# Performance work log

Hardware: AMD Instinct MI355X
Metric: run time of the kernel (lower is better)

Reference implementation:

```python
import jax, jax.numpy as jnp
import numpy as np

VEC_DIM = 64
RANK = 2


def setup_inputs() -> dict:
    key = jax.random.key(0)
    kg, km, kp = jax.random.split(key, 3)
    grid = jax.random.normal(kg, (193, 193, VEC_DIM), dtype=jnp.float32)
    # nn.init.uniform_(M.weight, -0.5, 0.5)
    M_weight = jax.random.uniform(km, (VEC_DIM, VEC_DIM), minval=-0.5, maxval=0.5, dtype=jnp.float32)
    # nn.init.uniform_(P, -0.1, 0.1)
    P = jax.random.uniform(kp, (VEC_DIM, VEC_DIM), minval=-0.1, maxval=0.1, dtype=jnp.float32)
    return {"grid": grid, "M_weight": M_weight, "P": P}


def reference(grid, M_weight, P):
    H, W, m = grid.shape
    # periods1[i,j] = periods2[i,j] = i*m + j + 2
    periods = (jnp.arange(m, dtype=jnp.float32)[:, None] * m
               + jnp.arange(m, dtype=jnp.float32)[None, :] + 2.0)  # [m, m]

    # ---- window extraction: linear mode (step=1), rank_mode='drop', rank_op='avg' ----
    nH = H - RANK + 1
    nW = W - RANK + 1
    win_sum = jax.lax.reduce_window(grid, 0.0, jax.lax.add,
                                    (RANK, RANK, 1), (1, 1, 1), 'VALID')  # [nH, nW, m]
    x_win = (win_sum / float(RANK * RANK)).reshape(nH * nW, m)  # [B, m]

    # ---- map through M (nn.Linear, no bias): y = x @ W^T ----
    x = x_win @ M_weight.T  # [B, m]

    # ---- phi_table gather: phi[k1,k2] = cos(2*pi*k1/periods) * cos(2*pi*k2/periods) ----
    two_pi = jnp.float32(2.0 * np.pi)
    k1s = jnp.arange(nH, dtype=jnp.float32)
    k2s = jnp.arange(nW, dtype=jnp.float32)
    cos1 = jnp.cos(two_pi * k1s[:, None, None] / periods)  # [nH, m, m]
    cos2 = jnp.cos(two_pi * k2s[:, None, None] / periods)  # [nW, m, m]
    phi = (cos1[:, None, :, :] * cos2[None, :, :, :]).reshape(nH * nW, m, m)  # [B, m, m]

    # ---- Nk = einsum('bj,ij,bij->bi', x, P, phi) ----
    Nk = jnp.einsum('bj,ij,bij->bi', x, P, phi)  # [B, m]
    return Nk
```

## Files before the change

kernel.cpp:

```cpp
#include <hip/hip_runtime.h>
#include <math.h>

#define NH 192
#define NW 192
#define Wt 193
#define TG 24
#define NTILE (TG*TG)
#define TILE_SZ 4096
#define TBLK 3072

__device__ __forceinline__ float cos_rev(float num, float den) {
    float rev = num * __builtin_amdgcn_rcpf(den);
    rev = __builtin_amdgcn_fractf(rev);
    return __builtin_amdgcn_cosf(rev);
}

__global__ __launch_bounds__(256) void k_prep(const float* __restrict__ grid,
                                              const float* __restrict__ Mw,
                                              const float* __restrict__ P,
                                              float* __restrict__ Cz,
                                              float* __restrict__ CP1,
                                              float* __restrict__ xt) {
    __shared__ float Ms[64 * 64];
    __shared__ float win[64 * 68];
    int bx = blockIdx.x;
    int t = threadIdx.x;

    if (bx < TBLK) {
        int idx = bx * 256 + t;
        int r  = idx & 3;
        int i  = (idx >> 2) & 63;
        int kg = (idx >> 8) % 48;
        int j  = idx / 12288;
        int k  = kg * 4 + r;
        Cz[idx] = cos_rev((float)k, (float)(i * 64 + j + 2));
        int i2 = idx & 63;
        int k2 = (idx >> 6) % 192;
        int j2 = idx / 12288;
        int t2 = i2 * 64 + j2;
        CP1[idx] = cos_rev((float)k2, (float)(t2 + 2)) * P[t2];
        return;
    }

    int bb = bx - TBLK;
    int k1g = bb % TG, k2g = bb / TG;

    #pragma unroll
    for (int r = 0; r < 4; ++r) {
        int e = r * 256 + t;
        ((float4*)Ms)[e] = ((const float4*)Mw)[e];
    }

    {
        int c = t & 63, pq = t >> 6;
        const float* gb = grid + ((size_t)(k1g * 8) * Wt + k2g * 8) * 64;
        #pragma unroll
        for (int r = 0; r < 16; ++r) {
            int p = pq * 16 + r;
            int l1 = p >> 3, l2 = p & 7;
            const float* g0 = gb + ((size_t)l1 * Wt + l2) * 64;
            float s = g0[c] + g0[64 + c] + g0[Wt * 64 + c] + g0[Wt * 64 + 64 + c];
            win[p * 68 + c] = 0.25f * s;
        }
    }
    __syncthreads();

    int p = t & 63, jq = t >> 6;
    float4 wv[16];
    #pragma unroll
    for (int q = 0; q < 16; ++q) wv[q] = *(const float4*)&win[p * 68 + 4 * q];

    float* xb = xt + (size_t)(k1g * TG + k2g) * TILE_SZ;
    #pragma unroll
    for (int r = 0; r < 16; ++r) {
        int j = jq * 16 + r;
        float acc = 0.f;
        #pragma unroll
        for (int q = 0; q < 16; ++q) {
            float4 mv = *(const float4*)&Ms[j * 64 + 4 * q];
            acc += wv[q].x * mv.x + wv[q].y * mv.y + wv[q].z * mv.z + wv[q].w * mv.w;
        }
        xb[(size_t)j * 64 + p] = acc;
    }
}

__global__ __launch_bounds__(512) void k_main(const float* __restrict__ xt,
                                              const float* __restrict__ Cz,
                                              const float* __restrict__ CP1,
                                              float* __restrict__ out) {
    __shared__ float4 cs[2048];
    int bx = blockIdx.x;
    int k1g = bx % TG, k2g = bx / TG;
    int t = threadIdx.x;
    int lane = t & 63;
    int w = __builtin_amdgcn_readfirstlane(t >> 6);
    int k1 = k1g * 8 + w;

    const float*  c1p = CP1 + (size_t)k1 * 64 + lane;
    const float*  xb  = xt + (size_t)(k1g * TG + k2g) * TILE_SZ + w * 8;
    const float4* Cz4 = (const float4*)Cz;
    int kgb = k2g * 2;

    float acc[8];
    #pragma unroll
    for (int l2 = 0; l2 < 8; ++l2) acc[l2] = 0.f;

    for (int jc = 0; jc < 4; ++jc) {
        __syncthreads();
        #pragma unroll
        for (int r = 0; r < 4; ++r) {
            int e = r * 512 + t;
            int jj = e >> 7;
            int g  = (e >> 6) & 1;
            int i  = e & 63;
            cs[e] = Cz4[(size_t)((jc * 16 + jj) * 48 + kgb + g) * 64 + i];
        }
        __syncthreads();

        #pragma unroll 4
        for (int jj = 0; jj < 16; ++jj) {
            int j = jc * 16 + jj;
            float  c1 = c1p[(size_t)j * 12288];
            float4 v0 = cs[jj * 128 + lane];
            float4 v1 = cs[jj * 128 + 64 + lane];
            const float4* xj = (const float4*)(xb + (size_t)j * 64);
            float4 x0 = xj[0];
            float4 x1 = xj[1];
            float c2f[8] = {v0.x, v0.y, v0.z, v0.w, v1.x, v1.y, v1.z, v1.w};
            float xs[8]  = {x0.x, x0.y, x0.z, x0.w, x1.x, x1.y, x1.z, x1.w};
            #pragma unroll
            for (int l2 = 0; l2 < 8; ++l2)
                acc[l2] += xs[l2] * (c1 * c2f[l2]);
        }
    }

    size_t ob = ((size_t)k1 * NW + k2g * 8) * 64 + lane;
    #pragma unroll
    for (int l2 = 0; l2 < 8; ++l2)
        out[ob + (size_t)l2 * 64] = acc[l2];
}

extern "C" void kernel_launch(void* const* d_in, const int* in_sizes, int n_in,
                              void* d_out, int out_size, void* d_ws, size_t ws_size,
                              hipStream_t stream) {
    const float* grid = (const float*)d_in[0];
    const float* Mw   = (const float*)d_in[1];
    const float* P    = (const float*)d_in[2];
    float* out = (float*)d_out;

    float* Cz  = (float*)d_ws;
    float* CP1 = Cz + 786432;
    float* xt  = CP1 + 786432;

    k_prep<<<TBLK + NTILE, 256, 0, stream>>>(grid, Mw, P, Cz, CP1, xt);
    k_main<<<NTILE, 512, 0, stream>>>(xt, Cz, CP1, out);
}
```

Baseline: 95.44 us.

## Split main kernel into 256-thread blocks and double-buffer cosine table staging

The main kernel now launches twice as many blocks with four waves each, so every block covers four k1 rows instead of eight. The Cz cosine slice is loaded in 8-row chunks into a double-buffered LDS array through registers, and the next chunk's global load is issued before the current chunk is computed. This overlaps global load latency with the FMA loop and halves the barriers per chunk. In exchange, each Cz chunk is loaded by twice as many blocks, raising total global and L2 traffic for that table.

```diff
diff --git a/kernel.cpp b/kernel.cpp
--- a/kernel.cpp
+++ b/kernel.cpp
@@ -6,6 +6,7 @@
 #define Wt 193
 #define TG 24
 #define NTILE (TG*TG)
+#define NMAIN 1152
 #define TILE_SZ 4096
 #define TBLK 3072
 
@@ -84,20 +85,21 @@
     }
 }
 
-__global__ __launch_bounds__(512) void k_main(const float* __restrict__ xt,
+__global__ __launch_bounds__(256) void k_main(const float* __restrict__ xt,
                                               const float* __restrict__ Cz,
                                               const float* __restrict__ CP1,
                                               float* __restrict__ out) {
     __shared__ float4 cs[2048];
     int bx = blockIdx.x;
-    int k1g = bx % TG, k2g = bx / TG;
+    int k1G = bx % 48, k2g = bx / 48;
     int t = threadIdx.x;
     int lane = t & 63;
     int w = __builtin_amdgcn_readfirstlane(t >> 6);
-    int k1 = k1g * 8 + w;
+    int k1 = k1G * 4 + w;
 
-    const float*  c1p = CP1 + (size_t)k1 * 64 + lane;
-    const float*  xb  = xt + (size_t)(k1g * TG + k2g) * TILE_SZ + w * 8;
+    const float* c1p = CP1 + (size_t)k1 * 64 + lane;
+    int wl = (k1G & 1) * 4 + w;
+    const float* xb = xt + (size_t)((k1G >> 1) * TG + k2g) * TILE_SZ + wl * 8;
     const float4* Cz4 = (const float4*)Cz;
     int kgb = k2g * 2;
 
@@ -105,24 +107,33 @@
     #pragma unroll
     for (int l2 = 0; l2 < 8; ++l2) acc[l2] = 0.f;
 
-    for (int jc = 0; jc < 4; ++jc) {
-        __syncthreads();
-        #pragma unroll
-        for (int r = 0; r < 4; ++r) {
-            int e = r * 512 + t;
-            int jj = e >> 7;
-            int g  = (e >> 6) & 1;
-            int i  = e & 63;
-            cs[e] = Cz4[(size_t)((jc * 16 + jj) * 48 + kgb + g) * 64 + i];
+    float4 stg[4];
+    #pragma unroll
+    for (int r = 0; r < 4; ++r) {
+        int e = r * 256 + t;
+        stg[r] = Cz4[(size_t)(((e >> 7)) * 48 + kgb + ((e >> 6) & 1)) * 64 + (e & 63)];
+    }
+    #pragma unroll
+    for (int r = 0; r < 4; ++r) cs[r * 256 + t] = stg[r];
+    __syncthreads();
+
+    for (int jc = 0; jc < 8; ++jc) {
+        int cur = jc & 1;
+        if (jc < 7) {
+            #pragma unroll
+            for (int r = 0; r < 4; ++r) {
+                int e = r * 256 + t;
+                stg[r] = Cz4[(size_t)(((jc + 1) * 8 + (e >> 7)) * 48 + kgb
+                                      + ((e >> 6) & 1)) * 64 + (e & 63)];
+            }
         }
-        __syncthreads();
 
         #pragma unroll 4
-        for (int jj = 0; jj < 16; ++jj) {
-            int j = jc * 16 + jj;
+        for (int jj = 0; jj < 8; ++jj) {
+            int j = jc * 8 + jj;
             float  c1 = c1p[(size_t)j * 12288];
-            float4 v0 = cs[jj * 128 + lane];
-            float4 v1 = cs[jj * 128 + 64 + lane];
+            float4 v0 = cs[cur * 1024 + jj * 128 + lane];
+            float4 v1 = cs[cur * 1024 + jj * 128 + 64 + lane];
             const float4* xj = (const float4*)(xb + (size_t)j * 64);
             float4 x0 = xj[0];
             float4 x1 = xj[1];
@@ -132,6 +143,13 @@
             for (int l2 = 0; l2 < 8; ++l2)
                 acc[l2] += xs[l2] * (c1 * c2f[l2]);
         }
+
+        if (jc < 7) {
+            #pragma unroll
+            for (int r = 0; r < 4; ++r)
+                cs[(cur ^ 1) * 1024 + r * 256 + t] = stg[r];
+        }
+        __syncthreads();
     }
 
     size_t ob = ((size_t)k1 * NW + k2g * 8) * 64 + lane;
@@ -153,5 +171,5 @@
     float* xt  = CP1 + 786432;
 
     k_prep<<<TBLK + NTILE, 256, 0, stream>>>(grid, Mw, P, Cz, CP1, xt);
-    k_main<<<NTILE, 512, 0, stream>>>(xt, Cz, CP1, out);
+    k_main<<<NMAIN, 256, 0, stream>>>(xt, Cz, CP1, out);
 }
```

Result: slower. 126.3 us (+32.3%).

## Replace precomputed cosine tables with on-the-fly Chebyshev recurrence in main kernel

Applied to the files above, without the earlier changes.

Drops the two large cosine/P tables written by the prep kernel and read back by the main kernel. The main kernel now computes cos(2πk2/T) along k2 with the Chebyshev recurrence c(k+1)=2cos(θ)c(k)-c(k-1), starting from two seeds per 16-wide chunk. The work is regridded to one k1 row and a 48-wide k2 chunk per block, with x staged transposed in LDS and partial sums reduced across waves through shared memory. This removes about 6 MB of table traffic and many transcendental evaluations, at the cost of extra FMAs, more LDS traffic and syncs, and possible accumulated rounding error from the recurrence.

```diff
diff --git a/kernel.cpp b/kernel.cpp
--- a/kernel.cpp
+++ b/kernel.cpp
@@ -7,42 +7,22 @@
 #define TG 24
 #define NTILE (TG*TG)
 #define TILE_SZ 4096
-#define TBLK 3072
+#define NMAIN 768
+#define CHUNK 48
 
-__device__ __forceinline__ float cos_rev(float num, float den) {
-    float rev = num * __builtin_amdgcn_rcpf(den);
+__device__ __forceinline__ float cos_revr(float num, float rcpden) {
+    float rev = num * rcpden;
     rev = __builtin_amdgcn_fractf(rev);
     return __builtin_amdgcn_cosf(rev);
 }
 
 __global__ __launch_bounds__(256) void k_prep(const float* __restrict__ grid,
                                               const float* __restrict__ Mw,
-                                              const float* __restrict__ P,
-                                              float* __restrict__ Cz,
-                                              float* __restrict__ CP1,
                                               float* __restrict__ xt) {
     __shared__ float Ms[64 * 64];
     __shared__ float win[64 * 68];
-    int bx = blockIdx.x;
+    int bb = blockIdx.x;
     int t = threadIdx.x;
-
-    if (bx < TBLK) {
-        int idx = bx * 256 + t;
-        int r  = idx & 3;
-        int i  = (idx >> 2) & 63;
-        int kg = (idx >> 8) % 48;
-        int j  = idx / 12288;
-        int k  = kg * 4 + r;
-        Cz[idx] = cos_rev((float)k, (float)(i * 64 + j + 2));
-        int i2 = idx & 63;
-        int k2 = (idx >> 6) % 192;
-        int j2 = idx / 12288;
-        int t2 = i2 * 64 + j2;
-        CP1[idx] = cos_rev((float)k2, (float)(t2 + 2)) * P[t2];
-        return;
-    }
-
-    int bb = bx - TBLK;
     int k1g = bb % TG, k2g = bb / TG;
 
     #pragma unroll
@@ -84,60 +64,110 @@
     }
 }
 
-__global__ __launch_bounds__(512) void k_main(const float* __restrict__ xt,
-                                              const float* __restrict__ Cz,
-                                              const float* __restrict__ CP1,
-                                              float* __restrict__ out) {
-    __shared__ float4 cs[2048];
+__global__ __launch_bounds__(256, 3) void k_main(const float* __restrict__ xt,
+                                                 const float* __restrict__ P,
+                                                 float* __restrict__ out) {
+    __shared__ float xls[CHUNK * 68];
+    __shared__ float pp[4096];
     int bx = blockIdx.x;
-    int k1g = bx % TG, k2g = bx / TG;
+    int k1 = bx >> 2;
+    int c  = bx & 3;
+    int k2s = c * CHUNK;
     int t = threadIdx.x;
     int lane = t & 63;
     int w = __builtin_amdgcn_readfirstlane(t >> 6);
-    int k1 = k1g * 8 + w;
+    int jb = w * 16;
 
-    const float*  c1p = CP1 + (size_t)k1 * 64 + lane;
-    const float*  xb  = xt + (size_t)(k1g * TG + k2g) * TILE_SZ + w * 8;
-    const float4* Cz4 = (const float4*)Cz;
-    int kgb = k2g * 2;
+    {
+        const float4* P4 = (const float4*)P;
+        #pragma unroll
+        for (int s = 0; s < 4; ++s) {
+            int e = s * 256 + t;
+            float4 v = P4[e];
+            int i = e >> 4, j0 = (e & 15) * 4;
+            pp[(j0 + 0) * 64 + i] = v.x;
+            pp[(j0 + 1) * 64 + i] = v.y;
+            pp[(j0 + 2) * 64 + i] = v.z;
+            pp[(j0 + 3) * 64 + i] = v.w;
+        }
+    }
+    {
+        int prow = k1 & 7;
+        const float4* xt4 = (const float4*)xt
+                          + (size_t)((k1 >> 3) * TG + c * 6) * (TILE_SZ / 4);
+        #pragma unroll
+        for (int s = 0; s < 3; ++s) {
+            int f = s * 256 + t;
+            int j = f / 12, u = f - 12 * j;
+            int tc = u >> 1, h = u & 1;
+            float4 v = xt4[tc * 1024 + j * 16 + prow * 2 + h];
+            int k2l = tc * 8 + h * 4;
+            xls[(k2l + 0) * 68 + j] = v.x;
+            xls[(k2l + 1) * 68 + j] = v.y;
+            xls[(k2l + 2) * 68 + j] = v.z;
+            xls[(k2l + 3) * 68 + j] = v.w;
+        }
+    }
+    __syncthreads();
 
-    float acc[8];
+    float A[16], c1v[16], ce[16], co[16];
     #pragma unroll
-    for (int l2 = 0; l2 < 8; ++l2) acc[l2] = 0.f;
+    for (int jl = 0; jl < 16; ++jl) {
+        float T  = (float)(lane * 64 + jb + jl + 2);
+        float rT = __builtin_amdgcn_rcpf(T);
+        A[jl]   = 2.0f * cos_revr(1.0f, rT);
+        c1v[jl] = cos_revr((float)k1, rT) * pp[(jb + jl) * 64 + lane];
+    }
+    __syncthreads();
 
-    for (int jc = 0; jc < 4; ++jc) {
+    float* part = pp;
+    for (int sub = 0; sub < 3; ++sub) {
+        int k2a = k2s + sub * 16;
+        #pragma unroll
+        for (int jl = 0; jl < 16; ++jl) {
+            float T  = (float)(lane * 64 + jb + jl + 2);
+            float rT = __builtin_amdgcn_rcpf(T);
+            ce[jl] = cos_revr((float)k2a, rT);
+            co[jl] = cos_revr((float)(k2a - 1), rT);
+        }
+        #pragma unroll
+        for (int nn = 0; nn < 8; ++nn) {
+            {
+                const float4* xq = (const float4*)&xls[(sub * 16 + 2 * nn) * 68 + jb];
+                float4 q0 = xq[0], q1 = xq[1], q2 = xq[2], q3 = xq[3];
+                float xs[16] = {q0.x, q0.y, q0.z, q0.w, q1.x, q1.y, q1.z, q1.w,
+                                q2.x, q2.y, q2.z, q2.w, q3.x, q3.y, q3.z, q3.w};
+                float psum = 0.f;
+                #pragma unroll
+                for (int jl = 0; jl < 16; ++jl) {
+                    psum   = fmaf(xs[jl] * c1v[jl], ce[jl], psum);
+                    co[jl] = fmaf(A[jl], ce[jl], -co[jl]);
+                }
+                part[(w * 16 + 2 * nn) * 64 + lane] = psum;
+            }
+            {
+                const float4* xq = (const float4*)&xls[(sub * 16 + 2 * nn + 1) * 68 + jb];
+                float4 q0 = xq[0], q1 = xq[1], q2 = xq[2], q3 = xq[3];
+                float xs[16] = {q0.x, q0.y, q0.z, q0.w, q1.x, q1.y, q1.z, q1.w,
+                                q2.x, q2.y, q2.z, q2.w, q3.x, q3.y, q3.z, q3.w};
+                float psum = 0.f;
+                #pragma unroll
+                for (int jl = 0; jl < 16; ++jl) {
+                    psum   = fmaf(xs[jl] * c1v[jl], co[jl], psum);
+                    ce[jl] = fmaf(A[jl], co[jl], -ce[jl]);
+                }
+                part[(w * 16 + 2 * nn + 1) * 64 + lane] = psum;
+            }
+        }
         __syncthreads();
         #pragma unroll
-        for (int r = 0; r < 4; ++r) {
-            int e = r * 512 + t;
-            int jj = e >> 7;
-            int g  = (e >> 6) & 1;
-            int i  = e & 63;
-            cs[e] = Cz4[(size_t)((jc * 16 + jj) * 48 + kgb + g) * 64 + i];
+        for (int s = 0; s < 4; ++s) {
+            int e = s * 256 + t;
+            float r = part[e] + part[1024 + e] + part[2048 + e] + part[3072 + e];
+            out[((size_t)k1 * NW + (k2a + (e >> 6))) * 64 + (e & 63)] = r;
         }
         __syncthreads();
-
-        #pragma unroll 4
-        for (int jj = 0; jj < 16; ++jj) {
-            int j = jc * 16 + jj;
-            float  c1 = c1p[(size_t)j * 12288];
-            float4 v0 = cs[jj * 128 + lane];
-            float4 v1 = cs[jj * 128 + 64 + lane];
-            const float4* xj = (const float4*)(xb + (size_t)j * 64);
-            float4 x0 = xj[0];
-            float4 x1 = xj[1];
-            float c2f[8] = {v0.x, v0.y, v0.z, v0.w, v1.x, v1.y, v1.z, v1.w};
-            float xs[8]  = {x0.x, x0.y, x0.z, x0.w, x1.x, x1.y, x1.z, x1.w};
-            #pragma unroll
-            for (int l2 = 0; l2 < 8; ++l2)
-                acc[l2] += xs[l2] * (c1 * c2f[l2]);
-        }
     }
-
-    size_t ob = ((size_t)k1 * NW + k2g * 8) * 64 + lane;
-    #pragma unroll
-    for (int l2 = 0; l2 < 8; ++l2)
-        out[ob + (size_t)l2 * 64] = acc[l2];
 }
 
 extern "C" void kernel_launch(void* const* d_in, const int* in_sizes, int n_in,
@@ -148,10 +178,8 @@
     const float* P    = (const float*)d_in[2];
     float* out = (float*)d_out;
 
-    float* Cz  = (float*)d_ws;
-    float* CP1 = Cz + 786432;
-    float* xt  = CP1 + 786432;
+    float* xt = (float*)d_ws;
 
-    k_prep<<<TBLK + NTILE, 256, 0, stream>>>(grid, Mw, P, Cz, CP1, xt);
-    k_main<<<NTILE, 512, 0, stream>>>(xt, Cz, CP1, out);
+    k_prep<<<NTILE, 256, 0, stream>>>(grid, Mw, xt);
+    k_main<<<NMAIN, 256, 0, stream>>>(xt, P, out);
 }
```

Result: no change. 95.41 us (-0.0%).
